# Optimization experiments

Measured on AMD Instinct MI355X. Metric: run time of the kernel, lower is better.

Reference implementation:

```python
import jax, jax.numpy as jnp
import numpy as np

N_EMBD = 1024
N_HEAD = 16
HEAD_DIM = N_EMBD // N_HEAD
NEG = -1e9


def setup_inputs() -> dict:
    key = jax.random.key(0)
    ks = jax.random.split(key, 5)
    B, S = 2, 2048
    x = jax.random.normal(ks[0], (B, S, N_EMBD), dtype=jnp.float32)
    # qkv_proj: Linear(n_embd, 3*n_embd) -> weight used as x @ W_qkv (W stored [in, out])
    scale = 1.0 / np.sqrt(N_EMBD)
    W_qkv = jax.random.normal(ks[1], (N_EMBD, 3 * N_EMBD), dtype=jnp.float32) * scale
    b_qkv = jax.random.normal(ks[2], (3 * N_EMBD,), dtype=jnp.float32) * 0.02
    W_out = jax.random.normal(ks[3], (N_EMBD, N_EMBD), dtype=jnp.float32) * scale
    b_out = jax.random.normal(ks[4], (N_EMBD,), dtype=jnp.float32) * 0.02
    return {"x": x, "W_qkv": W_qkv, "b_qkv": b_qkv, "W_out": W_out, "b_out": b_out}


def reference(x, W_qkv, b_qkv, W_out, b_out):
    B, S, E = x.shape
    qkv = x @ W_qkv + b_qkv                      # [B,S,3E]
    q, k, v = jnp.split(qkv, 3, axis=-1)
    # [B,S,E] -> [B,H,S,D]
    def split_heads(t):
        return t.reshape(B, S, N_HEAD, HEAD_DIM).transpose(0, 2, 1, 3)
    q, k, v = split_heads(q), split_heads(k), split_heads(v)
    scores = jnp.einsum("bhqd,bhkd->bhqk", q, k) / jnp.sqrt(jnp.float32(HEAD_DIM))
    causal = jnp.tril(jnp.ones((S, S), dtype=bool))
    scores = jnp.where(causal, scores, NEG)
    attn = jax.nn.softmax(scores, axis=-1)
    out = jnp.einsum("bhqk,bhkd->bhqd", attn, v)  # [B,H,S,D]
    out = out.transpose(0, 2, 1, 3).reshape(B, S, E)
    return out @ W_out + b_out
```

## Files before the change

### kernel.cpp

```cpp
#include <hip/hip_runtime.h>
#include <hip/hip_bf16.h>

#define BATCH 2
#define SEQ   2048
#define EMBD  1024
#define NHEAD 16
#define HDIM  64
#define QKV3  (3 * EMBD)

typedef __attribute__((ext_vector_type(8))) __bf16 bf16x8;
typedef __attribute__((ext_vector_type(4))) __bf16 bf16x4;
typedef __attribute__((ext_vector_type(4))) float f32x4;

__global__ __launch_bounds__(256) void cast_f32_bf16(
    const float* __restrict__ in, __bf16* __restrict__ out)
{
    int i = (blockIdx.x * 256 + threadIdx.x) * 8;
    float4 a = *(const float4*)&in[i];
    float4 b = *(const float4*)&in[i + 4];
    bf16x8 o;
    o[0] = (__bf16)a.x; o[1] = (__bf16)a.y; o[2] = (__bf16)a.z; o[3] = (__bf16)a.w;
    o[4] = (__bf16)b.x; o[5] = (__bf16)b.y; o[6] = (__bf16)b.z; o[7] = (__bf16)b.w;
    *(bf16x8*)&out[i] = o;
}

__global__ __launch_bounds__(256) void transpose_cast_bf16(
    const float* __restrict__ in, __bf16* __restrict__ out, int K, int N)
{
    __shared__ float t[64][65];
    const int k0 = blockIdx.y * 64, n0 = blockIdx.x * 64;
    const int tid = threadIdx.x;
    #pragma unroll
    for (int p = 0; p < 4; p++) {
        int kr = p * 16 + (tid >> 4);
        int c4 = (tid & 15) * 4;
        float4 v = *(const float4*)&in[(size_t)(k0 + kr) * N + n0 + c4];
        t[kr][c4] = v.x; t[kr][c4 + 1] = v.y; t[kr][c4 + 2] = v.z; t[kr][c4 + 3] = v.w;
    }
    __syncthreads();
    #pragma unroll
    for (int p = 0; p < 4; p++) {
        int nr = p * 16 + (tid >> 4);
        int k4 = (tid & 15) * 4;
        bf16x4 o;
        o[0] = (__bf16)t[k4 + 0][nr];
        o[1] = (__bf16)t[k4 + 1][nr];
        o[2] = (__bf16)t[k4 + 2][nr];
        o[3] = (__bf16)t[k4 + 3][nr];
        *(bf16x4*)&out[(size_t)(n0 + nr) * K + k0 + k4] = o;
    }
}

__global__ __launch_bounds__(256) void transpose_v_bf16(
    const __bf16* __restrict__ qkv, __bf16* __restrict__ vt)
{
    __shared__ __bf16 t[64][72];
    const int k0 = blockIdx.x * 64;
    const int bh = blockIdx.y;
    const int b = bh >> 4, h = bh & 15;
    const size_t base = (size_t)b * SEQ * QKV3 + 2 * EMBD + h * HDIM;
    const int tid = threadIdx.x;
    #pragma unroll
    for (int it = 0; it < 2; it++) {
        int flat = it * 256 + tid;
        int kr = flat >> 3;
        int d0 = (flat & 7) * 8;
        bf16x8 v = *(const bf16x8*)&qkv[base + (size_t)(k0 + kr) * QKV3 + d0];
        #pragma unroll
        for (int i = 0; i < 8; i++) t[kr][d0 + i] = v[i];
    }
    __syncthreads();
    #pragma unroll
    for (int it = 0; it < 2; it++) {
        int flat = it * 256 + tid;
        int d  = flat >> 3;
        int kc = (flat & 7) * 8;
        bf16x8 o;
        #pragma unroll
        for (int i = 0; i < 8; i++) o[i] = t[kc + i][d];
        *(bf16x8*)&vt[((size_t)bh * 64 + d) * SEQ + k0 + kc] = o;
    }
}

template<bool OUT_BF16>
__global__ __launch_bounds__(256) void gemm_bt_mfma(
    const __bf16* __restrict__ A,
    const __bf16* __restrict__ Bt,
    const float* __restrict__ bias,
    void* __restrict__ Cv,
    int M, int N, int K, int nscale)
{
    __shared__ __align__(16) __bf16 As[128 * 32];
    __shared__ __align__(16) __bf16 Bs[128 * 32];

    const int tid  = threadIdx.x;
    const int lane = tid & 63;
    const int wave = tid >> 6;
    const int wm = (wave >> 1) * 64;
    const int wn = (wave & 1) * 64;
    const int m0 = blockIdx.y * 128;
    const int n0 = blockIdx.x * 128;
    const int lm = lane & 15;
    const int kq = lane >> 4;

    f32x4 acc[4][4] = {};

    for (int k0 = 0; k0 < K; k0 += 32) {
        __syncthreads();
        #pragma unroll
        for (int r = 0; r < 2; r++) {
            int flat = r * 256 + tid;
            int row  = flat >> 2;
            int off  = (flat & 3) * 16;
            const char* ga = (const char*)(A + (size_t)(m0 + row) * K + k0) + off;
            char* la = (char*)As + flat * 16;
            __builtin_amdgcn_global_load_lds(
                (const __attribute__((address_space(1))) void*)ga,
                (__attribute__((address_space(3))) void*)la, 16, 0, 0);
            const char* gb = (const char*)(Bt + (size_t)(n0 + row) * K + k0) + off;
            char* lb = (char*)Bs + flat * 16;
            __builtin_amdgcn_global_load_lds(
                (const __attribute__((address_space(1))) void*)gb,
                (__attribute__((address_space(3))) void*)lb, 16, 0, 0);
        }
        __syncthreads();

        bf16x8 af[4], bf[4];
        #pragma unroll
        for (int t = 0; t < 4; t++) {
            af[t] = *(const bf16x8*)&As[(wm + t * 16 + lm) * 32 + kq * 8];
            bf[t] = *(const bf16x8*)&Bs[(wn + t * 16 + lm) * 32 + kq * 8];
        }
        #pragma unroll
        for (int i = 0; i < 4; i++)
            #pragma unroll
            for (int j = 0; j < 4; j++)
                acc[i][j] = __builtin_amdgcn_mfma_f32_16x16x32_bf16(
                    af[i], bf[j], acc[i][j], 0, 0, 0);
    }

    const int r0 = kq * 4;
    #pragma unroll
    for (int i = 0; i < 4; i++) {
        #pragma unroll
        for (int j = 0; j < 4; j++) {
            int col = n0 + wn + j * 16 + lm;
            float bv = bias[col];
            float sc = (col < nscale) ? 0.125f : 1.0f;
            #pragma unroll
            for (int r = 0; r < 4; r++) {
                int row = m0 + wm + i * 16 + r0 + r;
                float val = (acc[i][j][r] + bv) * sc;
                if (OUT_BF16) ((__bf16*)Cv)[(size_t)row * N + col] = (__bf16)val;
                else          ((float*)Cv)[(size_t)row * N + col] = val;
            }
        }
    }
}

__global__ __launch_bounds__(256) void attn_kpar_mfma(
    const __bf16* __restrict__ qkv, const __bf16* __restrict__ vt,
    __bf16* __restrict__ attn)
{
    __shared__ __align__(16) char smem[16896];

    const int tid  = threadIdx.x;
    const int wave = tid >> 6;
    const int lane = tid & 63;
    const int quad = lane >> 4;
    const int c    = lane & 15;

    const int bh = blockIdx.x;
    const int b  = bh >> 4;
    const int h  = bh & 15;
    const int qblk = (int)(gridDim.y - 1) - blockIdx.y;
    const int q0 = qblk * 32;

    const size_t base = (size_t)b * SEQ * QKV3;
    const int hoff = h * HDIM;
    const __bf16* vbase = vt + (size_t)bh * 64 * SEQ;

    bf16x8 aq[2][2];
    #pragma unroll
    for (int qf = 0; qf < 2; qf++) {
        const __bf16* qrow = qkv + base +
            (size_t)(q0 + qf * 16 + c) * QKV3 + hoff + quad * 8;
        aq[qf][0] = *(const bf16x8*)(qrow);
        aq[qf][1] = *(const bf16x8*)(qrow + 32);
    }

    f32x4 acc[2][4] = {};
    float lpart[2][4] = {};

    char* pbw = smem + wave * 4096;
    const int ntiles = q0 / 64 + 1;

    for (int t = wave; t < ntiles; t += 4) {
        const int k0 = t * 64;
        const bool diag = (t == ntiles - 1);

        #pragma unroll
        for (int jj = 0; jj < 4; jj++) {
            const __bf16* krow = qkv + base +
                (size_t)(k0 + jj * 16 + c) * QKV3 + EMBD + hoff + quad * 8;
            bf16x8 bk0 = *(const bf16x8*)(krow);
            bf16x8 bk1 = *(const bf16x8*)(krow + 32);
            const int kabs_c = k0 + jj * 16 + c;
            const int col = jj * 16 + c;
            const int ab = (col >> 5) * 1024 + ((col >> 3) & 3) * 256 + (col & 7) * 2;
            #pragma unroll
            for (int qf = 0; qf < 2; qf++) {
                f32x4 s = {};
                s = __builtin_amdgcn_mfma_f32_16x16x32_bf16(aq[qf][0], bk0, s, 0, 0, 0);
                s = __builtin_amdgcn_mfma_f32_16x16x32_bf16(aq[qf][1], bk1, s, 0, 0, 0);
                char* pq = pbw + qf * 2048 + ab;
                const int qabs0 = q0 + qf * 16 + quad * 4;
                #pragma unroll
                for (int r = 0; r < 4; r++) {
                    float p;
                    if (diag && (kabs_c > qabs0 + r)) p = 0.f;
                    else p = __expf(fminf(s[r], 60.f));
                    lpart[qf][r] += p;
                    *(__bf16*)(pq + (quad * 4 + r) * 16) = (__bf16)p;
                }
            }
        }

        bf16x8 ap[2][2];
        #pragma unroll
        for (int qf = 0; qf < 2; qf++) {
            ap[qf][0] = *(const bf16x8*)(pbw + qf * 2048 + lane * 16);
            ap[qf][1] = *(const bf16x8*)(pbw + qf * 2048 + 1024 + lane * 16);
        }

        #pragma unroll
        for (int dd = 0; dd < 4; dd++) {
            const __bf16* vr = vbase + (size_t)(dd * 16 + c) * SEQ + k0 + quad * 8;
            bf16x8 bv0 = *(const bf16x8*)(vr);
            bf16x8 bv1 = *(const bf16x8*)(vr + 32);
            #pragma unroll
            for (int qf = 0; qf < 2; qf++) {
                acc[qf][dd] = __builtin_amdgcn_mfma_f32_16x16x32_bf16(ap[qf][0], bv0, acc[qf][dd], 0, 0, 0);
                acc[qf][dd] = __builtin_amdgcn_mfma_f32_16x16x32_bf16(ap[qf][1], bv1, acc[qf][dd], 0, 0, 0);
            }
        }
    }

    #pragma unroll
    for (int qf = 0; qf < 2; qf++)
        #pragma unroll
        for (int r = 0; r < 4; r++) {
            float v = lpart[qf][r];
            v += __shfl_xor(v, 1);
            v += __shfl_xor(v, 2);
            v += __shfl_xor(v, 4);
            v += __shfl_xor(v, 8);
            lpart[qf][r] = v;
        }

    __syncthreads();

    float* Ored = (float*)smem;
    float* lred = (float*)(smem + 16640);

    if (wave < 2) {
        float* R = Ored + wave * (32 * 65);
        #pragma unroll
        for (int qf = 0; qf < 2; qf++)
            #pragma unroll
            for (int dd = 0; dd < 4; dd++)
                #pragma unroll
                for (int r = 0; r < 4; r++)
                    R[(qf * 16 + quad * 4 + r) * 65 + dd * 16 + c] = acc[qf][dd][r];
        if (c == 0) {
            #pragma unroll
            for (int qf = 0; qf < 2; qf++)
                #pragma unroll
                for (int r = 0; r < 4; r++)
                    lred[wave * 32 + qf * 16 + quad * 4 + r] = lpart[qf][r];
        }
    }
    __syncthreads();
    if (wave >= 2) {
        float* R = Ored + (wave - 2) * (32 * 65);
        #pragma unroll
        for (int qf = 0; qf < 2; qf++)
            #pragma unroll
            for (int dd = 0; dd < 4; dd++)
                #pragma unroll
                for (int r = 0; r < 4; r++)
                    R[(qf * 16 + quad * 4 + r) * 65 + dd * 16 + c] += acc[qf][dd][r];
        if (c == 0) {
            #pragma unroll
            for (int qf = 0; qf < 2; qf++)
                #pragma unroll
                for (int r = 0; r < 4; r++)
                    lred[(wave - 2) * 32 + qf * 16 + quad * 4 + r] += lpart[qf][r];
        }
    }
    __syncthreads();

    {
        const int row = tid >> 3;
        const int cg  = tid & 7;
        const float l = lred[row] + lred[32 + row];
        const float inv = 1.f / l;
        const float* R0 = Ored + row * 65 + cg * 8;
        const float* R1 = R0 + 32 * 65;
        bf16x8 o;
        #pragma unroll
        for (int i = 0; i < 8; i++) o[i] = (__bf16)((R0[i] + R1[i]) * inv);
        *(bf16x8*)&attn[((size_t)b * SEQ + q0 + row) * EMBD + hoff + cg * 8] = o;
    }
}

extern "C" void kernel_launch(void* const* d_in, const int* in_sizes, int n_in,
                              void* d_out, int out_size, void* d_ws, size_t ws_size,
                              hipStream_t stream)
{
    const float* x     = (const float*)d_in[0];
    const float* W_qkv = (const float*)d_in[1];
    const float* b_qkv = (const float*)d_in[2];
    const float* W_out = (const float*)d_in[3];
    const float* b_out = (const float*)d_in[4];
    float* out = (float*)d_out;

    const int M = BATCH * SEQ;

    __bf16* xbf    = (__bf16*)d_ws;
    __bf16* Wqkv_t = xbf    + (size_t)M * EMBD;
    __bf16* Wout_t = Wqkv_t + (size_t)QKV3 * EMBD;
    __bf16* qkv    = Wout_t + (size_t)EMBD * EMBD;
    __bf16* attn   = qkv    + (size_t)M * QKV3;
    __bf16* vtbuf  = attn   + (size_t)M * EMBD;

    cast_f32_bf16<<<(M * EMBD) / (256 * 8), 256, 0, stream>>>(x, xbf);
    {
        dim3 g(QKV3 / 64, EMBD / 64);
        transpose_cast_bf16<<<g, 256, 0, stream>>>(W_qkv, Wqkv_t, EMBD, QKV3);
    }
    {
        dim3 g(EMBD / 64, EMBD / 64);
        transpose_cast_bf16<<<g, 256, 0, stream>>>(W_out, Wout_t, EMBD, EMBD);
    }
    {
        dim3 grid(QKV3 / 128, M / 128);
        gemm_bt_mfma<true><<<grid, 256, 0, stream>>>(xbf, Wqkv_t, b_qkv, qkv, M, QKV3, EMBD, EMBD);
    }
    {
        dim3 grid(SEQ / 64, BATCH * NHEAD);
        transpose_v_bf16<<<grid, 256, 0, stream>>>(qkv, vtbuf);
    }
    {
        dim3 grid(BATCH * NHEAD, SEQ / 32);
        attn_kpar_mfma<<<grid, 256, 0, stream>>>(qkv, vtbuf, attn);
    }
    {
        dim3 grid(EMBD / 128, M / 128);
        gemm_bt_mfma<false><<<grid, 256, 0, stream>>>(attn, Wout_t, b_out, out, M, EMBD, EMBD, 0);
    }
}
```

Measured before the change: 222.4 us.

## Enlarge attention query tile to 64 rows, use exp2 with folded log2e scale

The attention kernel now handles 64 query rows per block instead of 32, so each loaded K and V tile is reused across four query fragments and the grid is halved. The softmax scale folds log2(e) into the Q projection so the kernel can call the hardware exp2 directly. The QK MFMA operands are swapped so each lane holds four consecutive keys, which allows packed bf16x4 stores of P and a cheaper row-sum reduction. The PV loop is split into two K-chunks under raised wave priority. In exchange the kernel uses more registers and double the shared memory, which may lower occupancy, and with half as many blocks the causal load imbalance is coarser.

```diff
diff --git a/kernel.cpp b/kernel.cpp
--- a/kernel.cpp
+++ b/kernel.cpp
@@ -8,9 +8,20 @@
 #define HDIM  64
 #define QKV3  (3 * EMBD)
 
+#define QSCALE 0.18033688011112042f
+#define SCLAMP 86.56f
+
 typedef __attribute__((ext_vector_type(8))) __bf16 bf16x8;
 typedef __attribute__((ext_vector_type(4))) __bf16 bf16x4;
 typedef __attribute__((ext_vector_type(4))) float f32x4;
+
+__device__ __forceinline__ float fast_exp2(float x) {
+#if __has_builtin(__builtin_amdgcn_exp2f)
+    return __builtin_amdgcn_exp2f(x);
+#else
+    return exp2f(x);
+#endif
+}
 
 __global__ __launch_bounds__(256) void cast_f32_bf16(
     const float* __restrict__ in, __bf16* __restrict__ out)
@@ -146,7 +157,7 @@
         for (int j = 0; j < 4; j++) {
             int col = n0 + wn + j * 16 + lm;
             float bv = bias[col];
-            float sc = (col < nscale) ? 0.125f : 1.0f;
+            float sc = (col < nscale) ? QSCALE : 1.0f;
             #pragma unroll
             for (int r = 0; r < 4; r++) {
                 int row = m0 + wm + i * 16 + r0 + r;
@@ -162,7 +173,7 @@
     const __bf16* __restrict__ qkv, const __bf16* __restrict__ vt,
     __bf16* __restrict__ attn)
 {
-    __shared__ __align__(16) char smem[16896];
+    __shared__ __align__(16) char smem[34304];
 
     const int tid  = threadIdx.x;
     const int wave = tid >> 6;
@@ -174,26 +185,26 @@
     const int b  = bh >> 4;
     const int h  = bh & 15;
     const int qblk = (int)(gridDim.y - 1) - blockIdx.y;
-    const int q0 = qblk * 32;
+    const int q0 = qblk * 64;
 
     const size_t base = (size_t)b * SEQ * QKV3;
     const int hoff = h * HDIM;
     const __bf16* vbase = vt + (size_t)bh * 64 * SEQ;
 
-    bf16x8 aq[2][2];
-    #pragma unroll
-    for (int qf = 0; qf < 2; qf++) {
+    bf16x8 aq[4][2];
+    #pragma unroll
+    for (int qf = 0; qf < 4; qf++) {
         const __bf16* qrow = qkv + base +
             (size_t)(q0 + qf * 16 + c) * QKV3 + hoff + quad * 8;
         aq[qf][0] = *(const bf16x8*)(qrow);
         aq[qf][1] = *(const bf16x8*)(qrow + 32);
     }
 
-    f32x4 acc[2][4] = {};
-    float lpart[2][4] = {};
-
-    char* pbw = smem + wave * 4096;
-    const int ntiles = q0 / 64 + 1;
+    f32x4 acc[4][4] = {};
+    float lpart[4] = {};
+
+    char* pbw = smem + wave * 8192;
+    const int ntiles = qblk + 1;
 
     for (int t = wave; t < ntiles; t += 4) {
         const int k0 = t * 64;
@@ -205,108 +216,98 @@
                 (size_t)(k0 + jj * 16 + c) * QKV3 + EMBD + hoff + quad * 8;
             bf16x8 bk0 = *(const bf16x8*)(krow);
             bf16x8 bk1 = *(const bf16x8*)(krow + 32);
-            const int kabs_c = k0 + jj * 16 + c;
-            const int col = jj * 16 + c;
-            const int ab = (col >> 5) * 1024 + ((col >> 3) & 3) * 256 + (col & 7) * 2;
-            #pragma unroll
-            for (int qf = 0; qf < 2; qf++) {
+            const int kb = k0 + jj * 16 + quad * 4;
+            const int wb = (jj >> 1) * 1024 + (((jj & 1) * 2 + (quad >> 1))) * 256
+                         + c * 16 + (quad & 1) * 8;
+            #pragma unroll
+            for (int qf = 0; qf < 4; qf++) {
                 f32x4 s = {};
-                s = __builtin_amdgcn_mfma_f32_16x16x32_bf16(aq[qf][0], bk0, s, 0, 0, 0);
-                s = __builtin_amdgcn_mfma_f32_16x16x32_bf16(aq[qf][1], bk1, s, 0, 0, 0);
-                char* pq = pbw + qf * 2048 + ab;
-                const int qabs0 = q0 + qf * 16 + quad * 4;
+                s = __builtin_amdgcn_mfma_f32_16x16x32_bf16(bk0, aq[qf][0], s, 0, 0, 0);
+                s = __builtin_amdgcn_mfma_f32_16x16x32_bf16(bk1, aq[qf][1], s, 0, 0, 0);
+                const int qa = q0 + qf * 16 + c;
+                bf16x4 pk;
                 #pragma unroll
                 for (int r = 0; r < 4; r++) {
                     float p;
-                    if (diag && (kabs_c > qabs0 + r)) p = 0.f;
-                    else p = __expf(fminf(s[r], 60.f));
-                    lpart[qf][r] += p;
-                    *(__bf16*)(pq + (quad * 4 + r) * 16) = (__bf16)p;
+                    if (diag && (kb + r > qa)) p = 0.f;
+                    else p = fast_exp2(fminf(s[r], SCLAMP));
+                    lpart[qf] += p;
+                    pk[r] = (__bf16)p;
                 }
+                *(bf16x4*)(pbw + qf * 2048 + wb) = pk;
             }
         }
 
-        bf16x8 ap[2][2];
-        #pragma unroll
-        for (int qf = 0; qf < 2; qf++) {
-            ap[qf][0] = *(const bf16x8*)(pbw + qf * 2048 + lane * 16);
-            ap[qf][1] = *(const bf16x8*)(pbw + qf * 2048 + 1024 + lane * 16);
-        }
-
-        #pragma unroll
-        for (int dd = 0; dd < 4; dd++) {
-            const __bf16* vr = vbase + (size_t)(dd * 16 + c) * SEQ + k0 + quad * 8;
-            bf16x8 bv0 = *(const bf16x8*)(vr);
-            bf16x8 bv1 = *(const bf16x8*)(vr + 32);
-            #pragma unroll
-            for (int qf = 0; qf < 2; qf++) {
-                acc[qf][dd] = __builtin_amdgcn_mfma_f32_16x16x32_bf16(ap[qf][0], bv0, acc[qf][dd], 0, 0, 0);
-                acc[qf][dd] = __builtin_amdgcn_mfma_f32_16x16x32_bf16(ap[qf][1], bv1, acc[qf][dd], 0, 0, 0);
+        __builtin_amdgcn_s_setprio(1);
+        #pragma unroll
+        for (int kc = 0; kc < 2; kc++) {
+            bf16x8 ap[4];
+            #pragma unroll
+            for (int qf = 0; qf < 4; qf++)
+                ap[qf] = *(const bf16x8*)(pbw + qf * 2048 + kc * 1024 + lane * 16);
+            #pragma unroll
+            for (int dd = 0; dd < 4; dd++) {
+                const __bf16* vr = vbase + (size_t)(dd * 16 + c) * SEQ
+                                 + k0 + kc * 32 + quad * 8;
+                bf16x8 bv = *(const bf16x8*)(vr);
+                #pragma unroll
+                for (int qf = 0; qf < 4; qf++)
+                    acc[qf][dd] = __builtin_amdgcn_mfma_f32_16x16x32_bf16(
+                        ap[qf], bv, acc[qf][dd], 0, 0, 0);
             }
         }
-    }
-
-    #pragma unroll
-    for (int qf = 0; qf < 2; qf++)
-        #pragma unroll
-        for (int r = 0; r < 4; r++) {
-            float v = lpart[qf][r];
-            v += __shfl_xor(v, 1);
-            v += __shfl_xor(v, 2);
-            v += __shfl_xor(v, 4);
-            v += __shfl_xor(v, 8);
-            lpart[qf][r] = v;
-        }
+        __builtin_amdgcn_s_setprio(0);
+    }
+
+    #pragma unroll
+    for (int qf = 0; qf < 4; qf++) {
+        float v = lpart[qf];
+        v += __shfl_xor(v, 16);
+        v += __shfl_xor(v, 32);
+        lpart[qf] = v;
+    }
 
     __syncthreads();
 
     float* Ored = (float*)smem;
-    float* lred = (float*)(smem + 16640);
+    float* lred = (float*)(smem + 33792);
 
     if (wave < 2) {
-        float* R = Ored + wave * (32 * 65);
-        #pragma unroll
-        for (int qf = 0; qf < 2; qf++)
+        float* R = Ored + wave * (64 * 66);
+        #pragma unroll
+        for (int qf = 0; qf < 4; qf++) {
             #pragma unroll
             for (int dd = 0; dd < 4; dd++)
                 #pragma unroll
                 for (int r = 0; r < 4; r++)
-                    R[(qf * 16 + quad * 4 + r) * 65 + dd * 16 + c] = acc[qf][dd][r];
-        if (c == 0) {
-            #pragma unroll
-            for (int qf = 0; qf < 2; qf++)
-                #pragma unroll
-                for (int r = 0; r < 4; r++)
-                    lred[wave * 32 + qf * 16 + quad * 4 + r] = lpart[qf][r];
+                    R[(qf * 16 + quad * 4 + r) * 66 + dd * 16 + c] = acc[qf][dd][r];
+            if (quad == 0) lred[wave * 64 + qf * 16 + c] = lpart[qf];
         }
     }
     __syncthreads();
     if (wave >= 2) {
-        float* R = Ored + (wave - 2) * (32 * 65);
-        #pragma unroll
-        for (int qf = 0; qf < 2; qf++)
+        float* R = Ored + (wave - 2) * (64 * 66);
+        #pragma unroll
+        for (int qf = 0; qf < 4; qf++) {
             #pragma unroll
             for (int dd = 0; dd < 4; dd++)
                 #pragma unroll
                 for (int r = 0; r < 4; r++)
-                    R[(qf * 16 + quad * 4 + r) * 65 + dd * 16 + c] += acc[qf][dd][r];
-        if (c == 0) {
-            #pragma unroll
-            for (int qf = 0; qf < 2; qf++)
-                #pragma unroll
-                for (int r = 0; r < 4; r++)
-                    lred[(wave - 2) * 32 + qf * 16 + quad * 4 + r] += lpart[qf][r];
-        }
-    }
-    __syncthreads();
-
-    {
-        const int row = tid >> 3;
-        const int cg  = tid & 7;
-        const float l = lred[row] + lred[32 + row];
+                    R[(qf * 16 + quad * 4 + r) * 66 + dd * 16 + c] += acc[qf][dd][r];
+            if (quad == 0) lred[(wave - 2) * 64 + qf * 16 + c] += lpart[qf];
+        }
+    }
+    __syncthreads();
+
+    #pragma unroll
+    for (int it = 0; it < 2; it++) {
+        const int flat = it * 256 + tid;
+        const int row = flat >> 3;
+        const int cg  = flat & 7;
+        const float l = lred[row] + lred[64 + row];
         const float inv = 1.f / l;
-        const float* R0 = Ored + row * 65 + cg * 8;
-        const float* R1 = R0 + 32 * 65;
+        const float* R0 = Ored + row * 66 + cg * 8;
+        const float* R1 = R0 + 64 * 66;
         bf16x8 o;
         #pragma unroll
         for (int i = 0; i < 8; i++) o[i] = (__bf16)((R0[i] + R1[i]) * inv);
@@ -352,7 +353,7 @@
         transpose_v_bf16<<<grid, 256, 0, stream>>>(qkv, vtbuf);
     }
     {
-        dim3 grid(BATCH * NHEAD, SEQ / 32);
+        dim3 grid(BATCH * NHEAD, SEQ / 64);
         attn_kpar_mfma<<<grid, 256, 0, stream>>>(qkv, vtbuf, attn);
     }
     {
```

After: 203.7 us. 1.09x faster.
